# Optimization experiments

Measured on AMD Instinct MI355X. Metric: run time of the kernel, lower is better.

The kernel has to match this reference:

```python
import jax, jax.numpy as jnp
import numpy as np

SCALE = 128.0  # init arg; divisor is sqrt(scale)
NEG_BIG = -1e10

def setup_inputs() -> dict:
    key = jax.random.key(0)
    kq, kk, kv, km = jax.random.split(key, 4)
    B, Nq, Nk, D = 16, 2048, 2048, 128
    q = jax.random.normal(kq, (B, Nq, D), dtype=jnp.float32)
    k = jax.random.normal(kk, (B, Nk, D), dtype=jnp.float32)
    v = jax.random.normal(kv, (B, Nk, D), dtype=jnp.float32)
    mask = jax.random.randint(km, (B, Nq, Nk), 0, 2).astype(bool)
    return {"q": q, "k": k, "v": v, "mask": mask}

def reference(q, k, v, mask):
    inv = 1.0 / np.sqrt(SCALE).astype(np.float32)
    # scores: [b, q, k]
    scores = jnp.einsum('bqd,bkd->bqk', q, k) * inv
    scores = jnp.where(mask, NEG_BIG, scores)
    att = jax.nn.softmax(scores, axis=-1)
    context = jnp.einsum('bqk,bkd->bqd', att, v)
    return (context, att)
```

## Files before the change

### kernel.cpp

```cpp
#include <hip/hip_runtime.h>

#define B_ 16
#define NQ 2048
#define NK 2048
#define DH 128
#define INV 0.08838834764831843f

typedef __attribute__((ext_vector_type(8))) short bf16x8;
typedef __attribute__((ext_vector_type(4))) float f32x4;

typedef const __attribute__((address_space(1))) unsigned int* gas1_t;
typedef __attribute__((address_space(3))) unsigned int* las3_t;

__device__ __forceinline__ unsigned short f2b(float f) {
  unsigned u = __float_as_uint(f);
  u += 0x7fff + ((u >> 16) & 1);
  return (unsigned short)(u >> 16);
}

__device__ __forceinline__ void gl_lds16(const unsigned short* g, unsigned short* l) {
  __builtin_amdgcn_global_load_lds((gas1_t)g, (las3_t)l, 16, 0, 0);
}

__global__ __launch_bounds__(256) void k_cvt(
    const float* __restrict__ src, unsigned short* __restrict__ dst, int n4) {
  int i = blockIdx.x * 256 + threadIdx.x;
  if (i >= n4) return;
  float4 f = ((const float4*)src)[i];
  ushort4 u;
  u.x = f2b(f.x); u.y = f2b(f.y); u.z = f2b(f.z); u.w = f2b(f.w);
  ((ushort4*)dst)[i] = u;
}

__global__ __launch_bounds__(256) void k_trans(
    const float* __restrict__ v, unsigned short* __restrict__ vt) {
  __shared__ float tile[32][33];
  const int b = blockIdx.z, kv0 = blockIdx.x << 5, d0 = blockIdx.y << 5;
  const int tx = threadIdx.x & 31, ty = threadIdx.x >> 5;
  #pragma unroll
  for (int i = 0; i < 4; i++)
    tile[ty + 8*i][tx] = v[((size_t)b*NK + kv0 + ty + 8*i)*DH + d0 + tx];
  __syncthreads();
  #pragma unroll
  for (int i = 0; i < 4; i++)
    vt[((size_t)b*DH + d0 + ty + 8*i)*NK + kv0 + tx] = f2b(tile[tx][ty + 8*i]);
}

__global__ __launch_bounds__(256, 4) void k_attn(
    const unsigned short* __restrict__ qb, const unsigned short* __restrict__ kb,
    const unsigned short* __restrict__ vtb, const int* __restrict__ mask,
    float* __restrict__ att, float* __restrict__ ctx) {
  __shared__ unsigned short KA[64*128];
  __shared__ unsigned short VA[128*64];
  __shared__ unsigned short Ps[32*64];
  __shared__ float Lrow[32];

  const int t = threadIdx.x;
  const int wave = t >> 6, lane = t & 63, quad = lane >> 4, l15 = lane & 15;
  const int rh = wave >> 1, nh = wave & 1;

  const int p = blockIdx.x + (blockIdx.y << 6);
  const int lid = ((p & 7) << 7) + (p >> 3);
  const int b = lid >> 6, q0 = (lid & 63) << 5;

  const unsigned short* qg = qb  + ((size_t)b*NQ + q0)*DH;
  const unsigned short* kg = kb  + (size_t)b*NK*DH;
  const unsigned short* vg = vtb + (size_t)b*DH*NK;
  const int* mg   = mask + ((size_t)b*NQ + q0)*NK;
  float*     attg = att  + ((size_t)b*NQ + q0)*NK;
  float*     cg   = ctx  + ((size_t)b*NQ + q0)*DH;

  if (t < 32) Lrow[t] = 0.f;

  bf16x8 qf[4];
  { const unsigned short* qr = qg + (size_t)(rh*16 + l15)*DH + quad*8;
    #pragma unroll
    for (int kd = 0; kd < 4; kd++) qf[kd] = *(const bf16x8*)(qr + kd*32); }

  const int row0 = rh*16 + quad*4;
  const int* mgR[4]; float* attR[4];
  #pragma unroll
  for (int r = 0; r < 4; r++) {
    mgR[r]  = mg   + (size_t)(row0 + r)*NK + nh*32 + l15;
    attR[r] = attg + (size_t)(row0 + r)*NK + nh*32 + l15;
  }

  const int kr0 = nh*32 + l15, kr1 = kr0 + 16;
  const int kbs0 = (kr0 << 8) ^ ((kr0 & 7) << 4);
  const int kbs1 = (kr1 << 8) ^ ((kr1 & 7) << 4);
  const int pr  = rh*16 + l15;
  const int pbs = (pr << 7) ^ ((pr & 7) << 4);
  int vbs[4];
  #pragma unroll
  for (int dt = 0; dt < 4; dt++) {
    int d = nh*64 + dt*16 + l15;
    vbs[dt] = (d << 7) ^ ((d & 7) << 4);
  }

  auto stageK = [&](unsigned short* buf, const unsigned short* src) {
    #pragma unroll
    for (int i = 0; i < 4; i++) {
      int L = (wave << 12) + (i << 10) + (lane << 4);
      int row = L >> 8;
      int cb  = (L & 255) ^ ((row & 7) << 4);
      gl_lds16(src + ((size_t)row << 7) + (cb >> 1), buf + (L >> 1));
    }
  };
  auto stageV = [&](const unsigned short* src) {
    #pragma unroll
    for (int i = 0; i < 4; i++) {
      int L = (wave << 12) + (i << 10) + (lane << 4);
      int d  = L >> 7;
      int cb = (L & 127) ^ ((d & 7) << 4);
      gl_lds16(src + (size_t)d*NK + (cb >> 1), VA + (L >> 1));
    }
  };
  auto loadMask = [&](int k0, int* mr) {
    #pragma unroll
    for (int nt = 0; nt < 2; nt++)
      #pragma unroll
      for (int r = 0; r < 4; r++)
        mr[nt*4 + r] = __builtin_nontemporal_load(mgR[r] + k0 + nt*16);
  };
  auto qkt = [&](const unsigned short* buf, f32x4& s0v, f32x4& s1v) {
    s0v = 0; s1v = 0;
    const char* bc = (const char*)buf;
    __builtin_amdgcn_s_setprio(1);
    #pragma unroll
    for (int kd = 0; kd < 4; kd++) {
      int cb = (kd*32 + quad*8) << 1;
      bf16x8 b0 = *(const bf16x8*)(bc + (kbs0 ^ cb));
      bf16x8 b1 = *(const bf16x8*)(bc + (kbs1 ^ cb));
      s0v = __builtin_amdgcn_mfma_f32_16x16x32_bf16(qf[kd], b0, s0v, 0, 0, 0);
      s1v = __builtin_amdgcn_mfma_f32_16x16x32_bf16(qf[kd], b1, s1v, 0, 0, 0);
    }
    __builtin_amdgcn_s_setprio(0);
  };

  unsigned mw0=0,mw1=0,mw2=0,mw3=0,mw4=0,mw5=0,mw6=0,mw7=0;
  float ls[4] = {0.f, 0.f, 0.f, 0.f};

  auto epi1 = [&](const int* mr, const f32x4& s0v, const f32x4& s1v) {
    unsigned nb = 0;
    #pragma unroll
    for (int nt = 0; nt < 2; nt++) {
      const f32x4& sv = nt ? s1v : s0v;
      #pragma unroll
      for (int r = 0; r < 4; r++) {
        float e = __expf(sv[r]*INV);
        if (mr[nt*4 + r] != 0) { nb |= 1u << (nt*4 + r); e = 0.f; }
        ls[r] += e;
      }
    }
    mw0=(mw0>>8)|(mw1<<24); mw1=(mw1>>8)|(mw2<<24); mw2=(mw2>>8)|(mw3<<24);
    mw3=(mw3>>8)|(mw4<<24); mw4=(mw4>>8)|(mw5<<24); mw5=(mw5>>8)|(mw6<<24);
    mw6=(mw6>>8)|(mw7<<24); mw7=(mw7>>8)|(nb<<24);
  };

  int mrA[8], mrB[8];
  stageK(KA, kg);
  loadMask(0, mrA);

  for (int t2 = 0; t2 < 32; t2 += 2) {
    __builtin_amdgcn_s_barrier();
    asm volatile("" ::: "memory");
    stageK(VA, kg + (size_t)(t2+1)*64*DH);
    loadMask((t2+1)*64, mrB);
    asm volatile("s_waitcnt vmcnt(12)" ::: "memory");
    __builtin_amdgcn_s_barrier();
    asm volatile("" ::: "memory");
    { f32x4 s0, s1; qkt(KA, s0, s1); epi1(mrA, s0, s1); }

    __builtin_amdgcn_s_barrier();
    asm volatile("" ::: "memory");
    if (t2 + 2 < 32) {
      stageK(KA, kg + (size_t)(t2+2)*64*DH);
      loadMask((t2+2)*64, mrA);
      asm volatile("s_waitcnt vmcnt(12)" ::: "memory");
    } else {
      asm volatile("s_waitcnt vmcnt(0)" ::: "memory");
    }
    __builtin_amdgcn_s_barrier();
    asm volatile("" ::: "memory");
    { f32x4 s0, s1; qkt(VA, s0, s1); epi1(mrB, s0, s1); }
  }

  __syncthreads();
  #pragma unroll
  for (int r = 0; r < 4; r++) atomicAdd(&Lrow[row0 + r], ls[r]);
  __syncthreads();
  float il[4];
  #pragma unroll
  for (int r = 0; r < 4; r++) il[r] = 1.0f / Lrow[row0 + r];

  f32x4 ca[4];
  #pragma unroll
  for (int dt = 0; dt < 4; dt++) ca[dt] = 0;

  stageK(KA, kg);
  for (int tt = 0; tt < 32; tt++) {
    __builtin_amdgcn_s_barrier();
    asm volatile("" ::: "memory");
    stageV(vg + tt*64);
    asm volatile("s_waitcnt vmcnt(4)" ::: "memory");
    __builtin_amdgcn_s_barrier();
    asm volatile("" ::: "memory");
    f32x4 s0, s1;
    qkt(KA, s0, s1);

    unsigned nb = mw0 & 255u;
    mw0=(mw0>>8)|(mw1<<24); mw1=(mw1>>8)|(mw2<<24); mw2=(mw2>>8)|(mw3<<24);
    mw3=(mw3>>8)|(mw4<<24); mw4=(mw4>>8)|(mw5<<24); mw5=(mw5>>8)|(mw6<<24);
    mw6=(mw6>>8)|(mw7<<24); mw7>>=8;
    #pragma unroll
    for (int nt = 0; nt < 2; nt++) {
      const f32x4& sv = nt ? s1 : s0;
      #pragma unroll
      for (int r = 0; r < 4; r++) {
        float e = __expf(sv[r]*INV) * il[r];
        if ((nb >> (nt*4 + r)) & 1) e = 0.f;
        attR[r][tt*64 + nt*16] = e;
        int row = row0 + r;
        int cbw = ((nh*32 + nt*16 + l15) << 1) ^ ((row & 7) << 4);
        *(unsigned short*)((char*)Ps + (row << 7) + cbw) = f2b(e);
      }
    }
    asm volatile("s_waitcnt vmcnt(8) lgkmcnt(0)" ::: "memory");
    __builtin_amdgcn_s_barrier();
    asm volatile("" ::: "memory");
    if (tt + 1 < 32) stageK(KA, kg + (size_t)(tt+1)*64*DH);

    __builtin_amdgcn_s_setprio(1);
    #pragma unroll
    for (int kv = 0; kv < 2; kv++) {
      int cb = (kv*32 + quad*8) << 1;
      bf16x8 pa = *(const bf16x8*)((const char*)Ps + (pbs ^ cb));
      #pragma unroll
      for (int dt = 0; dt < 4; dt++) {
        bf16x8 vb = *(const bf16x8*)((const char*)VA + (vbs[dt] ^ cb));
        ca[dt] = __builtin_amdgcn_mfma_f32_16x16x32_bf16(pa, vb, ca[dt], 0, 0, 0);
      }
    }
    __builtin_amdgcn_s_setprio(0);
  }

  #pragma unroll
  for (int dt = 0; dt < 4; dt++)
    #pragma unroll
    for (int r = 0; r < 4; r++)
      cg[(size_t)(row0 + r)*DH + nh*64 + dt*16 + l15] = ca[dt][r];
}

extern "C" void kernel_launch(void* const* d_in, const int* in_sizes, int n_in,
                              void* d_out, int out_size, void* d_ws, size_t ws_size,
                              hipStream_t stream) {
  const float* q = (const float*)d_in[0];
  const float* k = (const float*)d_in[1];
  const float* v = (const float*)d_in[2];
  const int* mask = (const int*)d_in[3];
  float* ctx = (float*)d_out;
  float* att = ctx + (size_t)B_*NQ*DH;

  const size_t NE = (size_t)B_*NQ*DH;
  unsigned short* qws = (unsigned short*)d_ws;
  unsigned short* kws = qws + NE;
  unsigned short* vws = kws + NE;

  k_cvt  <<<(int)(NE/1024), 256, 0, stream>>>(q, qws, (int)(NE/4));
  k_cvt  <<<(int)(NE/1024), 256, 0, stream>>>(k, kws, (int)(NE/4));
  k_trans<<<dim3(NK/32, DH/32, B_), 256, 0, stream>>>(v, vws);
  k_attn <<<dim3(NQ/32, B_), 256, 0, stream>>>(qws, kws, vws, mask, att, ctx);
}
```

Before: 572.8 us.

## Fold scale into Q, use exp2, unroll mask bit packing, shuffle-reduce row sums

Folds the 1/sqrt(d)·log2(e) factor into the Q bf16 conversion so the kernel can call the native exp2 without per-element multiplies. Unrolls the first pass by four tiles with four mask register sets, so the mask bitwords are packed once per four tiles instead of shifted through eight registers every tile. The row-sum reduction now uses wave shuffles before one atomic per 16 lanes, replacing per-lane LDS atomics. Scaling Q before bf16 rounding changes rounding slightly, and the extra mask buffers raise register pressure.

```diff
diff --git a/kernel.cpp b/kernel.cpp
--- a/kernel.cpp
+++ b/kernel.cpp
@@ -5,12 +5,16 @@
 #define NK 2048
 #define DH 128
 #define INV 0.08838834764831843f
+#define QSCALE (0.08838834764831843f * 1.4426950408889634f)
 
 typedef __attribute__((ext_vector_type(8))) short bf16x8;
 typedef __attribute__((ext_vector_type(4))) float f32x4;
 
 typedef const __attribute__((address_space(1))) unsigned int* gas1_t;
 typedef __attribute__((address_space(3))) unsigned int* las3_t;
+
+#define VMW(n)   asm volatile("s_waitcnt vmcnt(" #n ")" ::: "memory")
+#define BARRIER() do { __builtin_amdgcn_s_barrier(); asm volatile("" ::: "memory"); } while (0)
 
 __device__ __forceinline__ unsigned short f2b(float f) {
   unsigned u = __float_as_uint(f);
@@ -23,12 +27,14 @@
 }
 
 __global__ __launch_bounds__(256) void k_cvt(
-    const float* __restrict__ src, unsigned short* __restrict__ dst, int n4) {
+    const float* __restrict__ src, unsigned short* __restrict__ dst, int n4,
+    float scale) {
   int i = blockIdx.x * 256 + threadIdx.x;
   if (i >= n4) return;
   float4 f = ((const float4*)src)[i];
   ushort4 u;
-  u.x = f2b(f.x); u.y = f2b(f.y); u.z = f2b(f.z); u.w = f2b(f.w);
+  u.x = f2b(f.x * scale); u.y = f2b(f.y * scale);
+  u.z = f2b(f.z * scale); u.w = f2b(f.w * scale);
   ((ushort4*)dst)[i] = u;
 }
 
@@ -137,57 +143,67 @@
     __builtin_amdgcn_s_setprio(0);
   };
 
-  unsigned mw0=0,mw1=0,mw2=0,mw3=0,mw4=0,mw5=0,mw6=0,mw7=0;
   float ls[4] = {0.f, 0.f, 0.f, 0.f};
 
-  auto epi1 = [&](const int* mr, const f32x4& s0v, const f32x4& s1v) {
+  auto epi1 = [&](const int* mr, const f32x4& s0v, const f32x4& s1v) -> unsigned {
     unsigned nb = 0;
     #pragma unroll
     for (int nt = 0; nt < 2; nt++) {
       const f32x4& sv = nt ? s1v : s0v;
       #pragma unroll
       for (int r = 0; r < 4; r++) {
-        float e = __expf(sv[r]*INV);
+        float e = __builtin_amdgcn_exp2f(sv[r]);
         if (mr[nt*4 + r] != 0) { nb |= 1u << (nt*4 + r); e = 0.f; }
         ls[r] += e;
       }
     }
-    mw0=(mw0>>8)|(mw1<<24); mw1=(mw1>>8)|(mw2<<24); mw2=(mw2>>8)|(mw3<<24);
-    mw3=(mw3>>8)|(mw4<<24); mw4=(mw4>>8)|(mw5<<24); mw5=(mw5>>8)|(mw6<<24);
-    mw6=(mw6>>8)|(mw7<<24); mw7=(mw7>>8)|(nb<<24);
-  };
-
-  int mrA[8], mrB[8];
-  stageK(KA, kg);
-  loadMask(0, mrA);
-
-  for (int t2 = 0; t2 < 32; t2 += 2) {
-    __builtin_amdgcn_s_barrier();
-    asm volatile("" ::: "memory");
-    stageK(VA, kg + (size_t)(t2+1)*64*DH);
-    loadMask((t2+1)*64, mrB);
-    asm volatile("s_waitcnt vmcnt(12)" ::: "memory");
-    __builtin_amdgcn_s_barrier();
-    asm volatile("" ::: "memory");
-    { f32x4 s0, s1; qkt(KA, s0, s1); epi1(mrA, s0, s1); }
-
-    __builtin_amdgcn_s_barrier();
-    asm volatile("" ::: "memory");
-    if (t2 + 2 < 32) {
-      stageK(KA, kg + (size_t)(t2+2)*64*DH);
-      loadMask((t2+2)*64, mrA);
-      asm volatile("s_waitcnt vmcnt(12)" ::: "memory");
-    } else {
-      asm volatile("s_waitcnt vmcnt(0)" ::: "memory");
-    }
-    __builtin_amdgcn_s_barrier();
-    asm volatile("" ::: "memory");
-    { f32x4 s0, s1; qkt(VA, s0, s1); epi1(mrB, s0, s1); }
-  }
+    return nb;
+  };
+
+  unsigned mw0=0,mw1=0,mw2=0,mw3=0,mw4=0,mw5=0,mw6=0,mw7=0;
+
+  int mrA[8], mrB[8], mrC[8], mrD[8];
+  stageK(KA, kg);                 loadMask(0,    mrA);
+  stageK(VA, kg + (size_t)64*DH); loadMask(64,   mrB);
+
+#define S1_STEP(RDBUF, MR, SH, VN) do {                                  \
+    VMW(VN); BARRIER();                                                  \
+    f32x4 s0, s1; qkt(RDBUF, s0, s1);                                    \
+    bw |= epi1(MR, s0, s1) << SH;                                        \
+    BARRIER(); } while (0)
+
+  for (int t2 = 0; t2 < 28; t2 += 4) {
+    unsigned bw = 0;
+    S1_STEP(KA, mrA, 0, 12);
+    stageK(KA, kg + (size_t)(t2+2)*64*DH); loadMask((t2+2)*64, mrC);
+    S1_STEP(VA, mrB, 8, 12);
+    stageK(VA, kg + (size_t)(t2+3)*64*DH); loadMask((t2+3)*64, mrD);
+    S1_STEP(KA, mrC, 16, 12);
+    stageK(KA, kg + (size_t)(t2+4)*64*DH); loadMask((t2+4)*64, mrA);
+    S1_STEP(VA, mrD, 24, 12);
+    stageK(VA, kg + (size_t)(t2+5)*64*DH); loadMask((t2+5)*64, mrB);
+    mw0=mw1; mw1=mw2; mw2=mw3; mw3=mw4; mw4=mw5; mw5=mw6; mw6=mw7; mw7=bw;
+  }
+  {
+    unsigned bw = 0;
+    S1_STEP(KA, mrA, 0, 12);
+    stageK(KA, kg + (size_t)30*64*DH); loadMask(30*64, mrC);
+    S1_STEP(VA, mrB, 8, 12);
+    stageK(VA, kg + (size_t)31*64*DH); loadMask(31*64, mrD);
+    S1_STEP(KA, mrC, 16, 12);
+    S1_STEP(VA, mrD, 24, 0);
+    mw0=mw1; mw1=mw2; mw2=mw3; mw3=mw4; mw4=mw5; mw5=mw6; mw6=mw7; mw7=bw;
+  }
+#undef S1_STEP
 
   __syncthreads();
   #pragma unroll
-  for (int r = 0; r < 4; r++) atomicAdd(&Lrow[row0 + r], ls[r]);
+  for (int r = 0; r < 4; r++) {
+    float v = ls[r];
+    v += __shfl_xor(v, 1); v += __shfl_xor(v, 2);
+    v += __shfl_xor(v, 4); v += __shfl_xor(v, 8);
+    if (l15 == 0) atomicAdd(&Lrow[row0 + r], v);
+  }
   __syncthreads();
   float il[4];
   #pragma unroll
@@ -198,50 +214,50 @@
   for (int dt = 0; dt < 4; dt++) ca[dt] = 0;
 
   stageK(KA, kg);
-  for (int tt = 0; tt < 32; tt++) {
-    __builtin_amdgcn_s_barrier();
-    asm volatile("" ::: "memory");
-    stageV(vg + tt*64);
-    asm volatile("s_waitcnt vmcnt(4)" ::: "memory");
-    __builtin_amdgcn_s_barrier();
-    asm volatile("" ::: "memory");
-    f32x4 s0, s1;
-    qkt(KA, s0, s1);
-
-    unsigned nb = mw0 & 255u;
-    mw0=(mw0>>8)|(mw1<<24); mw1=(mw1>>8)|(mw2<<24); mw2=(mw2>>8)|(mw3<<24);
-    mw3=(mw3>>8)|(mw4<<24); mw4=(mw4>>8)|(mw5<<24); mw5=(mw5>>8)|(mw6<<24);
-    mw6=(mw6>>8)|(mw7<<24); mw7>>=8;
-    #pragma unroll
-    for (int nt = 0; nt < 2; nt++) {
-      const f32x4& sv = nt ? s1 : s0;
-      #pragma unroll
-      for (int r = 0; r < 4; r++) {
-        float e = __expf(sv[r]*INV) * il[r];
-        if ((nb >> (nt*4 + r)) & 1) e = 0.f;
-        attR[r][tt*64 + nt*16] = e;
-        int row = row0 + r;
-        int cbw = ((nh*32 + nt*16 + l15) << 1) ^ ((row & 7) << 4);
-        *(unsigned short*)((char*)Ps + (row << 7) + cbw) = f2b(e);
+  for (int t4 = 0; t4 < 32; t4 += 4) {
+    unsigned cw = mw0;
+    mw0=mw1; mw1=mw2; mw2=mw3; mw3=mw4; mw4=mw5; mw5=mw6; mw6=mw7;
+    #pragma unroll
+    for (int k = 0; k < 4; k++) {
+      const int tt = t4 + k;
+      BARRIER();
+      stageV(vg + tt*64);
+      VMW(4);
+      BARRIER();
+      f32x4 s0, s1;
+      qkt(KA, s0, s1);
+
+      const unsigned nb = (cw >> (8*k)) & 255u;
+      #pragma unroll
+      for (int nt = 0; nt < 2; nt++) {
+        const f32x4& sv = nt ? s1 : s0;
+        #pragma unroll
+        for (int r = 0; r < 4; r++) {
+          float e = __builtin_amdgcn_exp2f(sv[r]) * il[r];
+          if ((nb >> (nt*4 + r)) & 1) e = 0.f;
+          attR[r][tt*64 + nt*16] = e;
+          int row = row0 + r;
+          int cbw = ((nh*32 + nt*16 + l15) << 1) ^ ((row & 7) << 4);
+          *(unsigned short*)((char*)Ps + (row << 7) + cbw) = f2b(e);
+        }
       }
-    }
-    asm volatile("s_waitcnt vmcnt(8) lgkmcnt(0)" ::: "memory");
-    __builtin_amdgcn_s_barrier();
-    asm volatile("" ::: "memory");
-    if (tt + 1 < 32) stageK(KA, kg + (size_t)(tt+1)*64*DH);
-
-    __builtin_amdgcn_s_setprio(1);
-    #pragma unroll
-    for (int kv = 0; kv < 2; kv++) {
-      int cb = (kv*32 + quad*8) << 1;
-      bf16x8 pa = *(const bf16x8*)((const char*)Ps + (pbs ^ cb));
-      #pragma unroll
-      for (int dt = 0; dt < 4; dt++) {
-        bf16x8 vb = *(const bf16x8*)((const char*)VA + (vbs[dt] ^ cb));
-        ca[dt] = __builtin_amdgcn_mfma_f32_16x16x32_bf16(pa, vb, ca[dt], 0, 0, 0);
+      asm volatile("s_waitcnt vmcnt(8) lgkmcnt(0)" ::: "memory");
+      BARRIER();
+      if (tt + 1 < 32) stageK(KA, kg + (size_t)(tt+1)*64*DH);
+
+      __builtin_amdgcn_s_setprio(1);
+      #pragma unroll
+      for (int kv = 0; kv < 2; kv++) {
+        int cb = (kv*32 + quad*8) << 1;
+        bf16x8 pa = *(const bf16x8*)((const char*)Ps + (pbs ^ cb));
+        #pragma unroll
+        for (int dt = 0; dt < 4; dt++) {
+          bf16x8 vb = *(const bf16x8*)((const char*)VA + (vbs[dt] ^ cb));
+          ca[dt] = __builtin_amdgcn_mfma_f32_16x16x32_bf16(pa, vb, ca[dt], 0, 0, 0);
+        }
       }
-    }
-    __builtin_amdgcn_s_setprio(0);
+      __builtin_amdgcn_s_setprio(0);
+    }
   }
 
   #pragma unroll
@@ -266,8 +282,8 @@
   unsigned short* kws = qws + NE;
   unsigned short* vws = kws + NE;
 
-  k_cvt  <<<(int)(NE/1024), 256, 0, stream>>>(q, qws, (int)(NE/4));
-  k_cvt  <<<(int)(NE/1024), 256, 0, stream>>>(k, kws, (int)(NE/4));
+  k_cvt  <<<(int)(NE/1024), 256, 0, stream>>>(q, qws, (int)(NE/4), QSCALE);
+  k_cvt  <<<(int)(NE/1024), 256, 0, stream>>>(k, kws, (int)(NE/4), 1.0f);
   k_trans<<<dim3(NK/32, DH/32, B_), 256, 0, stream>>>(v, vws);
   k_attn <<<dim3(NQ/32, B_), 256, 0, stream>>>(qws, kws, vws, mask, att, ctx);
 }
```

Measured after the change: 582.0 us. Within noise of the previous version (+1.6%).
